# Kernel optimization log

Hardware: AMD Instinct MI355X
Metric: run time of the kernel (lower is better)

The kernel has to match this reference:

```python
import jax, jax.numpy as jnp
import numpy as np

N, IN, H, C, E = 20000, 256, 256, 16, 640000

def sage_conv(x, edge_index, W_l, b_l, W_r):
    # PyG SAGEConv (aggr='mean', root_weight=True):
    # out = lin_l(mean_{j in N(i)} x_j) + lin_r(x_i)
    src, dst = edge_index[0], edge_index[1]
    n = x.shape[0]
    msgs = x[src]                                            # [E, d] irregular gather
    agg = jax.ops.segment_sum(msgs, dst, num_segments=n)     # [N, d]
    deg = jax.ops.segment_sum(jnp.ones((msgs.shape[0],), x.dtype), dst, num_segments=n)
    agg = agg / jnp.maximum(deg, 1.0)[:, None]               # mean aggregation
    return agg @ W_l + b_l + x @ W_r


def setup_inputs() -> dict:
    key = jax.random.key(0)
    ks = jax.random.split(key, 10)
    s = lambda k, fi, fo: jax.random.normal(k, (fi, fo), jnp.float32) / np.sqrt(fi)
    return {
        "x": jax.random.normal(ks[0], (N, IN), jnp.float32),
        "edge_index": jax.random.randint(ks[1], (2, E), 0, N, jnp.int64),
        "W1l": s(ks[2], IN, H), "b1": jnp.zeros((H,), jnp.float32), "W1r": s(ks[3], IN, H),
        "W2l": s(ks[4], H, H),  "b2": jnp.zeros((H,), jnp.float32), "W2r": s(ks[5], H, H),
        "Wc": s(ks[6], H, C),   "bc": jnp.zeros((C,), jnp.float32),
    }


def reference(x, edge_index, W1l, b1, W1r, W2l, b2, W2r, Wc, bc):
    h = sage_conv(x, edge_index, W1l, b1, W1r)
    h = jax.nn.relu(h)                    # dropout is identity in eval mode
    z = sage_conv(h, edge_index, W2l, b2, W2r)
    return z @ Wc + bc                    # classifier logits [N, C]
```

## Files before the change

### kernel.cpp

```cpp
#include <hip/hip_runtime.h>
#include <hip/hip_bf16.h>


#define FEAT 256
#define NCLS 16
#define ZPAD 264
#define CAP  128

typedef __bf16 bf16x8 __attribute__((ext_vector_type(8)));
typedef __bf16 bf16x4 __attribute__((ext_vector_type(4)));
typedef float  f32x4  __attribute__((ext_vector_type(4)));
typedef float  f32x2  __attribute__((ext_vector_type(2)));
typedef unsigned int uint4v __attribute__((ext_vector_type(4)));


__global__ void combo_kernel(const float* __restrict__ x,
                             const float* __restrict__ W1l, const float* __restrict__ W1r,
                             const float* __restrict__ W2l, const float* __restrict__ W2r,
                             const float* __restrict__ Wc, const float* __restrict__ b2,
                             const float* __restrict__ bc,
                             const int* __restrict__ src, const int* __restrict__ dst,
                             __bf16* __restrict__ xb, unsigned char* __restrict__ x8,
                             __bf16* __restrict__ W1lT, __bf16* __restrict__ W1rT,
                             __bf16* __restrict__ WaT, __bf16* __restrict__ WbT,
                             float* __restrict__ bc2,
                             int* __restrict__ cnt, unsigned short* __restrict__ bucket,
                             int n4, int E, int nb_cvt) {
    int t = threadIdx.x;
    int bx = blockIdx.x;
    if (bx < nb_cvt) {
        int i = bx * 256 + t;
        if (i < n4) {
            f32x4 v = ((const f32x4*)x)[i];
            bf16x4 o;
            #pragma unroll
            for (int j = 0; j < 4; ++j) o[j] = (__bf16)v[j];
            ((bf16x4*)xb)[i] = o;
            int pk = 0;
            pk = __builtin_amdgcn_cvt_pk_fp8_f32(v[0], v[1], pk, false);
            pk = __builtin_amdgcn_cvt_pk_fp8_f32(v[2], v[3], pk, true);
            ((int*)x8)[i] = pk;
        }
    } else if (bx < nb_cvt + 512) {
        int b = bx - nb_cvt;
        int w = b >> 8, nn = b & 255;
        const float* W = w ? W1r : W1l;
        __bf16* WT = w ? W1rT : W1lT;
        WT[nn * FEAT + t] = (__bf16)W[t * FEAT + nn];
    } else if (bx < nb_cvt + 512 + 32) {
        int b = bx - nb_cvt - 512;
        int c = b & 15;
        const float* W = (b < 16) ? W2l : W2r;
        __bf16* WT = (b < 16) ? WaT : WbT;
        float s = 0.f;
        #pragma unroll 4
        for (int m = 0; m < FEAT; ++m)
            s += W[t * FEAT + m] * Wc[m * NCLS + c];
        WT[c * FEAT + t] = (__bf16)s;
    } else if (bx == nb_cvt + 512 + 32) {
        if (t < NCLS) {
            float s = 0.f;
            for (int k = 0; k < FEAT; ++k) s += b2[k] * Wc[k * NCLS + t];
            bc2[t] = s + bc[t];
        }
    } else {
        int idx = (bx - nb_cvt - 512 - 33) * 256 + t;
        int e2 = idx * 2;
        if (e2 < E) {
            int2 sv = *(const int2*)(src + e2);
            int2 dv = *(const int2*)(dst + e2);
            int p0 = atomicAdd(&cnt[dv.x], 1);
            if (p0 < CAP) bucket[dv.x * CAP + p0] = (unsigned short)sv.x;
            if (e2 + 1 < E) {
                int p1 = atomicAdd(&cnt[dv.y], 1);
                if (p1 < CAP) bucket[dv.y * CAP + p1] = (unsigned short)sv.y;
            }
        }
    }
}


__global__ __launch_bounds__(256) void agg_fp8_kernel(
    const unsigned char* __restrict__ t8, const int* __restrict__ cnt,
    const unsigned short* __restrict__ bucket, __bf16* __restrict__ out, int n)
{
    int wave = threadIdx.x >> 6;
    int node = blockIdx.x * 4 + wave;
    if (node >= n) return;
    int lane = threadIdx.x & 63;
    int quad = lane >> 4, l16 = lane & 15;
    int c = cnt[node];
    int deg = c < CAP ? c : CAP;
    const unsigned short* lst = bucket + node * CAP;

    f32x4 s0[4], s1[4];
    #pragma unroll
    for (int w = 0; w < 4; ++w) { s0[w] = (f32x4){0.f,0.f,0.f,0.f}; s1[w] = (f32x4){0.f,0.f,0.f,0.f}; }

    int e = quad;
    for (; e + 4 < deg; e += 8) {
        int j0 = lst[e], j1 = lst[e + 4];
        uint4v u0 = *(const uint4v*)(t8 + (size_t)j0 * FEAT + l16 * 16);
        uint4v u1 = *(const uint4v*)(t8 + (size_t)j1 * FEAT + l16 * 16);
        #pragma unroll
        for (int w = 0; w < 4; ++w) {
            f32x2 lo0 = __builtin_amdgcn_cvt_pk_f32_fp8(u0[w], false);
            f32x2 hi0 = __builtin_amdgcn_cvt_pk_f32_fp8(u0[w], true);
            s0[w][0] += lo0[0]; s0[w][1] += lo0[1]; s0[w][2] += hi0[0]; s0[w][3] += hi0[1];
            f32x2 lo1 = __builtin_amdgcn_cvt_pk_f32_fp8(u1[w], false);
            f32x2 hi1 = __builtin_amdgcn_cvt_pk_f32_fp8(u1[w], true);
            s1[w][0] += lo1[0]; s1[w][1] += lo1[1]; s1[w][2] += hi1[0]; s1[w][3] += hi1[1];
        }
    }
    if (e < deg) {
        int j = lst[e];
        uint4v u = *(const uint4v*)(t8 + (size_t)j * FEAT + l16 * 16);
        #pragma unroll
        for (int w = 0; w < 4; ++w) {
            f32x2 lo = __builtin_amdgcn_cvt_pk_f32_fp8(u[w], false);
            f32x2 hi = __builtin_amdgcn_cvt_pk_f32_fp8(u[w], true);
            s0[w][0] += lo[0]; s0[w][1] += lo[1]; s0[w][2] += hi[0]; s0[w][3] += hi[1];
        }
    }

    #pragma unroll
    for (int w = 0; w < 4; ++w)
        #pragma unroll
        for (int j = 0; j < 4; ++j) {
            float v = s0[w][j] + s1[w][j];
            v += __shfl_xor(v, 16, 64);
            v += __shfl_xor(v, 32, 64);
            s0[w][j] = v;
        }

    float inv = (c > 0) ? 1.0f / (float)c : 0.0f;
    bf16x4 o;
    #pragma unroll
    for (int j = 0; j < 4; ++j) o[j] = (__bf16)(s0[quad][j] * inv);
    *(bf16x4*)(out + (size_t)node * FEAT + l16 * 16 + quad * 4) = o;
}


__global__ __launch_bounds__(256) void gemm1_kernel(
    const __bf16* __restrict__ A1, const __bf16* __restrict__ A2,
    const __bf16* __restrict__ B1T, const __bf16* __restrict__ B2T,
    const float* __restrict__ bias,
    const __bf16* __restrict__ WaT, const __bf16* __restrict__ WbT,
    const float* __restrict__ bc2,
    __bf16* __restrict__ pb, float* __restrict__ q, int M)
{
    __shared__ __align__(16) __bf16 tile[32][ZPAD];

    int m0   = blockIdx.x * 32;
    int lane = threadIdx.x & 63;
    int wave = threadIdx.x >> 6;
    int l16  = lane & 15, quad = lane >> 4;

    f32x4 acc[2][4];
    #pragma unroll
    for (int a = 0; a < 2; ++a)
        #pragma unroll
        for (int b = 0; b < 4; ++b) acc[a][b] = (f32x4){0.f, 0.f, 0.f, 0.f};

    int arow[2];
    #pragma unroll
    for (int mt = 0; mt < 2; ++mt) {
        int r = m0 + mt * 16 + l16;
        arow[mt] = (r < M) ? r : (M - 1);
    }
    int nbase = wave * 64;

    for (int pass = 0; pass < 2; ++pass) {
        const __bf16* A  = pass ? A2 : A1;
        const __bf16* BT = pass ? B2T : B1T;
        #pragma unroll 2
        for (int kk = 0; kk < 8; ++kk) {
            int k0 = kk * 32 + quad * 8;
            bf16x8 af[2], bfm[4];
            #pragma unroll
            for (int mt = 0; mt < 2; ++mt)
                af[mt] = *(const bf16x8*)(A + (size_t)arow[mt] * FEAT + k0);
            #pragma unroll
            for (int nt = 0; nt < 4; ++nt)
                bfm[nt] = *(const bf16x8*)(BT + (size_t)(nbase + nt * 16 + l16) * FEAT + k0);
            #pragma unroll
            for (int mt = 0; mt < 2; ++mt)
                #pragma unroll
                for (int nt = 0; nt < 4; ++nt)
                    acc[mt][nt] = __builtin_amdgcn_mfma_f32_16x16x32_bf16(
                        af[mt], bfm[nt], acc[mt][nt], 0, 0, 0);
        }
    }

    #pragma unroll
    for (int nt = 0; nt < 4; ++nt) {
        int col = nbase + nt * 16 + l16;
        float bv = bias[col];
        #pragma unroll
        for (int mt = 0; mt < 2; ++mt) {
            int lr = mt * 16 + quad * 4;
            #pragma unroll
            for (int r = 0; r < 4; ++r) {
                float v = acc[mt][nt][r] + bv;
                tile[lr + r][col] = (__bf16)(v > 0.f ? v : 0.f);
            }
        }
    }
    __syncthreads();

    if (wave < 2) {
        int lr = wave * 16 + l16;
        f32x4 ap = {0.f, 0.f, 0.f, 0.f}, aq = {0.f, 0.f, 0.f, 0.f};
        #pragma unroll
        for (int kk = 0; kk < 8; ++kk) {
            int k0 = kk * 32 + quad * 8;
            bf16x8 a  = *(const bf16x8*)(&tile[lr][k0]);
            bf16x8 ba = *(const bf16x8*)(WaT + (size_t)l16 * FEAT + k0);
            bf16x8 bb = *(const bf16x8*)(WbT + (size_t)l16 * FEAT + k0);
            ap = __builtin_amdgcn_mfma_f32_16x16x32_bf16(a, ba, ap, 0, 0, 0);
            aq = __builtin_amdgcn_mfma_f32_16x16x32_bf16(a, bb, aq, 0, 0, 0);
        }
        float qv = bc2[l16];
        #pragma unroll
        for (int r = 0; r < 4; ++r) {
            int row = m0 + wave * 16 + quad * 4 + r;
            if (row < M) {
                pb[(size_t)row * NCLS + l16] = (__bf16)ap[r];
                q[(size_t)row * NCLS + l16] = aq[r] + qv;
            }
        }
    }
}


__global__ __launch_bounds__(256) void agg_out_kernel(
    const __bf16* __restrict__ pb, const float* __restrict__ q,
    const int* __restrict__ cnt, const unsigned short* __restrict__ bucket,
    float* __restrict__ out, int n)
{
    int wave = threadIdx.x >> 6;
    int node = blockIdx.x * 4 + wave;
    if (node >= n) return;
    int lane = threadIdx.x & 63;
    int quad = lane >> 4, l16 = lane & 15;
    int c = cnt[node];
    int deg = c < CAP ? c : CAP;
    const unsigned short* lst = bucket + node * CAP;

    float s0 = 0.f, s1 = 0.f;
    int e = quad;
    for (; e + 4 < deg; e += 8) {
        int j0 = lst[e], j1 = lst[e + 4];
        s0 += (float)pb[(size_t)j0 * NCLS + l16];
        s1 += (float)pb[(size_t)j1 * NCLS + l16];
    }
    if (e < deg) s0 += (float)pb[(size_t)lst[e] * NCLS + l16];

    float v = s0 + s1;
    v += __shfl_xor(v, 16, 64);
    v += __shfl_xor(v, 32, 64);

    if (quad == 0) {
        float inv = (c > 0) ? 1.0f / (float)c : 0.0f;
        out[(size_t)node * NCLS + l16] = v * inv + q[(size_t)node * NCLS + l16];
    }
}


extern "C" void kernel_launch(void* const* d_in, const int* in_sizes, int n_in,
                              void* d_out, int out_size, void* d_ws, size_t ws_size,
                              hipStream_t stream) {
    const float* x   = (const float*)d_in[0];
    const int*   ei  = (const int*)d_in[1];
    const float* W1l = (const float*)d_in[2];
    const float* b1  = (const float*)d_in[3];
    const float* W1r = (const float*)d_in[4];
    const float* W2l = (const float*)d_in[5];
    const float* b2  = (const float*)d_in[6];
    const float* W2r = (const float*)d_in[7];
    const float* Wc  = (const float*)d_in[8];
    const float* bc  = (const float*)d_in[9];
    float* out = (float*)d_out;

    const int n = in_sizes[0] / FEAT;
    const int E = in_sizes[1] / 2;
    const int* srcp = ei;
    const int* dstp = ei + E;

    char* p = (char*)d_ws;
    auto alloc = [&](size_t bytes) { char* r = p; p += (bytes + 511) & ~511ull; return r; };
    int* cnt       = (int*)alloc((size_t)n * 4);
    unsigned short* bucket = (unsigned short*)alloc((size_t)n * CAP * 2);
    __bf16* W1lT   = (__bf16*)alloc((size_t)FEAT * FEAT * 2);
    __bf16* W1rT   = (__bf16*)alloc((size_t)FEAT * FEAT * 2);
    __bf16* WaT    = (__bf16*)alloc((size_t)NCLS * FEAT * 2);
    __bf16* WbT    = (__bf16*)alloc((size_t)NCLS * FEAT * 2);
    float*  bc2    = (float*)alloc((size_t)NCLS * 4);
    __bf16* xb     = (__bf16*)alloc((size_t)n * FEAT * 2);
    unsigned char* x8 = (unsigned char*)alloc((size_t)n * FEAT);
    __bf16* aggb   = (__bf16*)alloc((size_t)n * FEAT * 2);
    __bf16* pb     = (__bf16*)alloc((size_t)n * NCLS * 2);
    float*  qb     = (float*)alloc((size_t)n * NCLS * 4);

    int n4 = n * FEAT / 4;
    int nb_cvt = (n4 + 255) / 256;
    int nb_edge = (E + 511) / 512;

    hipMemsetAsync(cnt, 0, (size_t)n * 4, stream);

    combo_kernel<<<nb_cvt + 512 + 32 + 1 + nb_edge, 256, 0, stream>>>(
        x, W1l, W1r, W2l, W2r, Wc, b2, bc, srcp, dstp,
        xb, x8, W1lT, W1rT, WaT, WbT, bc2, cnt, bucket, n4, E, nb_cvt);

    agg_fp8_kernel<<<(n + 3) / 4, 256, 0, stream>>>(x8, cnt, bucket, aggb, n);
    gemm1_kernel<<<(n + 31) / 32, 256, 0, stream>>>(aggb, xb, W1lT, W1rT, b1,
                                                    WaT, WbT, bc2, pb, qb, n);

    agg_out_kernel<<<(n + 3) / 4, 256, 0, stream>>>(pb, qb, cnt, bucket, out, n);
}
```

Measured before the change: 199.5 us.

## Reorder combo blocks, vectorize edge bucketing, prefetch neighbor lists via shuffles

The edge-bucketing blocks now come first in the combo kernel and each thread handles four edges with int4 loads and nontemporal bucket stores. Both aggregation kernels load the whole neighbor list once per wave into registers and hand indices out with wave shuffles, unrolling four gathers per iteration for more loads in flight. The tail GEMM epilogue spreads the two 16-class projections across all four waves instead of two. The aim is to cut dependent index-load latency and idle waves, at the cost of extra shuffle instructions and more branches.

After: 214.0 us. 1.07x slower.

```diff
diff --git a/kernel.cpp b/kernel.cpp
--- a/kernel.cpp
+++ b/kernel.cpp
@@ -12,6 +12,15 @@
 typedef float  f32x4  __attribute__((ext_vector_type(4)));
 typedef float  f32x2  __attribute__((ext_vector_type(2)));
 typedef unsigned int uint4v __attribute__((ext_vector_type(4)));
+
+#define ACC8(S, U) do {                                                   \
+    _Pragma("unroll")                                                     \
+    for (int w_ = 0; w_ < 4; ++w_) {                                      \
+        f32x2 lo_ = __builtin_amdgcn_cvt_pk_f32_fp8(U[w_], false);        \
+        f32x2 hi_ = __builtin_amdgcn_cvt_pk_f32_fp8(U[w_], true);         \
+        S[w_][0] += lo_[0]; S[w_][1] += lo_[1];                           \
+        S[w_][2] += hi_[0]; S[w_][3] += hi_[1];                           \
+    } } while (0)
 
 
 __global__ void combo_kernel(const float* __restrict__ x,
@@ -25,11 +34,31 @@
                              __bf16* __restrict__ WaT, __bf16* __restrict__ WbT,
                              float* __restrict__ bc2,
                              int* __restrict__ cnt, unsigned short* __restrict__ bucket,
-                             int n4, int E, int nb_cvt) {
+                             int n4, int E, int nb_edge, int nb_cvt) {
     int t = threadIdx.x;
     int bx = blockIdx.x;
-    if (bx < nb_cvt) {
-        int i = bx * 256 + t;
+    if (bx < nb_edge) {
+        int e4 = (bx * 256 + t) * 4;
+        if (((E & 3) == 0) && e4 + 3 < E) {
+            int4 sv = *(const int4*)(src + e4);
+            int4 dv = *(const int4*)(dst + e4);
+            int p0 = atomicAdd(&cnt[dv.x], 1);
+            int p1 = atomicAdd(&cnt[dv.y], 1);
+            int p2 = atomicAdd(&cnt[dv.z], 1);
+            int p3 = atomicAdd(&cnt[dv.w], 1);
+            if (p0 < CAP) __builtin_nontemporal_store((unsigned short)sv.x, &bucket[(size_t)dv.x * CAP + p0]);
+            if (p1 < CAP) __builtin_nontemporal_store((unsigned short)sv.y, &bucket[(size_t)dv.y * CAP + p1]);
+            if (p2 < CAP) __builtin_nontemporal_store((unsigned short)sv.z, &bucket[(size_t)dv.z * CAP + p2]);
+            if (p3 < CAP) __builtin_nontemporal_store((unsigned short)sv.w, &bucket[(size_t)dv.w * CAP + p3]);
+        } else {
+            for (int k = 0; k < 4 && e4 + k < E; ++k) {
+                int s = src[e4 + k], d = dst[e4 + k];
+                int p = atomicAdd(&cnt[d], 1);
+                if (p < CAP) __builtin_nontemporal_store((unsigned short)s, &bucket[(size_t)d * CAP + p]);
+            }
+        }
+    } else if (bx < nb_edge + nb_cvt) {
+        int i = (bx - nb_edge) * 256 + t;
         if (i < n4) {
             f32x4 v = ((const f32x4*)x)[i];
             bf16x4 o;
@@ -41,14 +70,14 @@
             pk = __builtin_amdgcn_cvt_pk_fp8_f32(v[2], v[3], pk, true);
             ((int*)x8)[i] = pk;
         }
-    } else if (bx < nb_cvt + 512) {
-        int b = bx - nb_cvt;
+    } else if (bx < nb_edge + nb_cvt + 512) {
+        int b = bx - nb_edge - nb_cvt;
         int w = b >> 8, nn = b & 255;
         const float* W = w ? W1r : W1l;
         __bf16* WT = w ? W1rT : W1lT;
         WT[nn * FEAT + t] = (__bf16)W[t * FEAT + nn];
-    } else if (bx < nb_cvt + 512 + 32) {
-        int b = bx - nb_cvt - 512;
+    } else if (bx < nb_edge + nb_cvt + 512 + 32) {
+        int b = bx - nb_edge - nb_cvt - 512;
         int c = b & 15;
         const float* W = (b < 16) ? W2l : W2r;
         __bf16* WT = (b < 16) ? WaT : WbT;
@@ -57,24 +86,11 @@
         for (int m = 0; m < FEAT; ++m)
             s += W[t * FEAT + m] * Wc[m * NCLS + c];
         WT[c * FEAT + t] = (__bf16)s;
-    } else if (bx == nb_cvt + 512 + 32) {
+    } else {
         if (t < NCLS) {
             float s = 0.f;
             for (int k = 0; k < FEAT; ++k) s += b2[k] * Wc[k * NCLS + t];
             bc2[t] = s + bc[t];
-        }
-    } else {
-        int idx = (bx - nb_cvt - 512 - 33) * 256 + t;
-        int e2 = idx * 2;
-        if (e2 < E) {
-            int2 sv = *(const int2*)(src + e2);
-            int2 dv = *(const int2*)(dst + e2);
-            int p0 = atomicAdd(&cnt[dv.x], 1);
-            if (p0 < CAP) bucket[dv.x * CAP + p0] = (unsigned short)sv.x;
-            if (e2 + 1 < E) {
-                int p1 = atomicAdd(&cnt[dv.y], 1);
-                if (p1 < CAP) bucket[dv.y * CAP + p1] = (unsigned short)sv.y;
-            }
         }
     }
 }
@@ -93,33 +109,44 @@
     int deg = c < CAP ? c : CAP;
     const unsigned short* lst = bucket + node * CAP;
 
+    int e0 = 0, e1 = 0;
+    if (lane < deg)      e0 = lst[lane];
+    if (lane + 64 < deg) e1 = lst[lane + 64];
+
     f32x4 s0[4], s1[4];
     #pragma unroll
     for (int w = 0; w < 4; ++w) { s0[w] = (f32x4){0.f,0.f,0.f,0.f}; s1[w] = (f32x4){0.f,0.f,0.f,0.f}; }
 
-    int e = quad;
-    for (; e + 4 < deg; e += 8) {
-        int j0 = lst[e], j1 = lst[e + 4];
-        uint4v u0 = *(const uint4v*)(t8 + (size_t)j0 * FEAT + l16 * 16);
-        uint4v u1 = *(const uint4v*)(t8 + (size_t)j1 * FEAT + l16 * 16);
-        #pragma unroll
-        for (int w = 0; w < 4; ++w) {
-            f32x2 lo0 = __builtin_amdgcn_cvt_pk_f32_fp8(u0[w], false);
-            f32x2 hi0 = __builtin_amdgcn_cvt_pk_f32_fp8(u0[w], true);
-            s0[w][0] += lo0[0]; s0[w][1] += lo0[1]; s0[w][2] += hi0[0]; s0[w][3] += hi0[1];
-            f32x2 lo1 = __builtin_amdgcn_cvt_pk_f32_fp8(u1[w], false);
-            f32x2 hi1 = __builtin_amdgcn_cvt_pk_f32_fp8(u1[w], true);
-            s1[w][0] += lo1[0]; s1[w][1] += lo1[1]; s1[w][2] += hi1[0]; s1[w][3] += hi1[1];
-        }
-    }
-    if (e < deg) {
-        int j = lst[e];
-        uint4v u = *(const uint4v*)(t8 + (size_t)j * FEAT + l16 * 16);
-        #pragma unroll
-        for (int w = 0; w < 4; ++w) {
-            f32x2 lo = __builtin_amdgcn_cvt_pk_f32_fp8(u[w], false);
-            f32x2 hi = __builtin_amdgcn_cvt_pk_f32_fp8(u[w], true);
-            s0[w][0] += lo[0]; s0[w][1] += lo[1]; s0[w][2] += hi[0]; s0[w][3] += hi[1];
+    int nfull = deg >> 2;
+    int rem   = deg & 3;
+    const unsigned char* base = t8 + l16 * 16;
+
+    int tt = 0;
+    for (; tt + 3 < nfull; tt += 4) {
+        int i0 = (tt + 0) * 4 + quad, i1 = (tt + 1) * 4 + quad;
+        int i2 = (tt + 2) * 4 + quad, i3 = (tt + 3) * 4 + quad;
+        int j0 = (i0 < 64) ? __shfl(e0, i0) : __shfl(e1, i0 - 64);
+        int j1 = (i1 < 64) ? __shfl(e0, i1) : __shfl(e1, i1 - 64);
+        int j2 = (i2 < 64) ? __shfl(e0, i2) : __shfl(e1, i2 - 64);
+        int j3 = (i3 < 64) ? __shfl(e0, i3) : __shfl(e1, i3 - 64);
+        uint4v u0 = *(const uint4v*)(base + (size_t)j0 * FEAT);
+        uint4v u1 = *(const uint4v*)(base + (size_t)j1 * FEAT);
+        uint4v u2 = *(const uint4v*)(base + (size_t)j2 * FEAT);
+        uint4v u3 = *(const uint4v*)(base + (size_t)j3 * FEAT);
+        ACC8(s0, u0); ACC8(s1, u1); ACC8(s0, u2); ACC8(s1, u3);
+    }
+    for (; tt < nfull; ++tt) {
+        int i = tt * 4 + quad;
+        int j = (i < 64) ? __shfl(e0, i) : __shfl(e1, i - 64);
+        uint4v u = *(const uint4v*)(base + (size_t)j * FEAT);
+        ACC8(s0, u);
+    }
+    if (rem) {
+        int i = nfull * 4 + quad;
+        int j = (i < 64) ? __shfl(e0, i) : __shfl(e1, i - 64);
+        if (quad < rem) {
+            uint4v u = *(const uint4v*)(base + (size_t)j * FEAT);
+            ACC8(s1, u);
         }
     }
 
@@ -208,25 +235,30 @@
     }
     __syncthreads();
 
-    if (wave < 2) {
-        int lr = wave * 16 + l16;
-        f32x4 ap = {0.f, 0.f, 0.f, 0.f}, aq = {0.f, 0.f, 0.f, 0.f};
+    {
+        int half = wave >> 1;
+        int lr = half * 16 + l16;
+        const __bf16* WT = (wave & 1) ? WbT : WaT;
+        f32x4 a = {0.f, 0.f, 0.f, 0.f};
         #pragma unroll
         for (int kk = 0; kk < 8; ++kk) {
             int k0 = kk * 32 + quad * 8;
-            bf16x8 a  = *(const bf16x8*)(&tile[lr][k0]);
-            bf16x8 ba = *(const bf16x8*)(WaT + (size_t)l16 * FEAT + k0);
-            bf16x8 bb = *(const bf16x8*)(WbT + (size_t)l16 * FEAT + k0);
-            ap = __builtin_amdgcn_mfma_f32_16x16x32_bf16(a, ba, ap, 0, 0, 0);
-            aq = __builtin_amdgcn_mfma_f32_16x16x32_bf16(a, bb, aq, 0, 0, 0);
-        }
-        float qv = bc2[l16];
-        #pragma unroll
-        for (int r = 0; r < 4; ++r) {
-            int row = m0 + wave * 16 + quad * 4 + r;
-            if (row < M) {
-                pb[(size_t)row * NCLS + l16] = (__bf16)ap[r];
-                q[(size_t)row * NCLS + l16] = aq[r] + qv;
+            bf16x8 av = *(const bf16x8*)(&tile[lr][k0]);
+            bf16x8 bv = *(const bf16x8*)(WT + (size_t)l16 * FEAT + k0);
+            a = __builtin_amdgcn_mfma_f32_16x16x32_bf16(av, bv, a, 0, 0, 0);
+        }
+        if (wave & 1) {
+            float qv = bc2[l16];
+            #pragma unroll
+            for (int r = 0; r < 4; ++r) {
+                int row = m0 + half * 16 + quad * 4 + r;
+                if (row < M) q[(size_t)row * NCLS + l16] = a[r] + qv;
+            }
+        } else {
+            #pragma unroll
+            for (int r = 0; r < 4; ++r) {
+                int row = m0 + half * 16 + quad * 4 + r;
+                if (row < M) pb[(size_t)row * NCLS + l16] = (__bf16)a[r];
             }
         }
     }
@@ -247,14 +279,39 @@
     int deg = c < CAP ? c : CAP;
     const unsigned short* lst = bucket + node * CAP;
 
+    int e0 = 0, e1 = 0;
+    if (lane < deg)      e0 = lst[lane];
+    if (lane + 64 < deg) e1 = lst[lane + 64];
+
     float s0 = 0.f, s1 = 0.f;
-    int e = quad;
-    for (; e + 4 < deg; e += 8) {
-        int j0 = lst[e], j1 = lst[e + 4];
-        s0 += (float)pb[(size_t)j0 * NCLS + l16];
-        s1 += (float)pb[(size_t)j1 * NCLS + l16];
-    }
-    if (e < deg) s0 += (float)pb[(size_t)lst[e] * NCLS + l16];
+    int nfull = deg >> 2;
+    int rem   = deg & 3;
+
+    int tt = 0;
+    for (; tt + 3 < nfull; tt += 4) {
+        int i0 = (tt + 0) * 4 + quad, i1 = (tt + 1) * 4 + quad;
+        int i2 = (tt + 2) * 4 + quad, i3 = (tt + 3) * 4 + quad;
+        int j0 = (i0 < 64) ? __shfl(e0, i0) : __shfl(e1, i0 - 64);
+        int j1 = (i1 < 64) ? __shfl(e0, i1) : __shfl(e1, i1 - 64);
+        int j2 = (i2 < 64) ? __shfl(e0, i2) : __shfl(e1, i2 - 64);
+        int j3 = (i3 < 64) ? __shfl(e0, i3) : __shfl(e1, i3 - 64);
+        float v0 = (float)pb[(size_t)j0 * NCLS + l16];
+        float v1 = (float)pb[(size_t)j1 * NCLS + l16];
+        float v2 = (float)pb[(size_t)j2 * NCLS + l16];
+        float v3 = (float)pb[(size_t)j3 * NCLS + l16];
+        s0 += v0 + v1;
+        s1 += v2 + v3;
+    }
+    for (; tt < nfull; ++tt) {
+        int i = tt * 4 + quad;
+        int j = (i < 64) ? __shfl(e0, i) : __shfl(e1, i - 64);
+        s0 += (float)pb[(size_t)j * NCLS + l16];
+    }
+    if (rem) {
+        int i = nfull * 4 + quad;
+        int j = (i < 64) ? __shfl(e0, i) : __shfl(e1, i - 64);
+        if (quad < rem) s1 += (float)pb[(size_t)j * NCLS + l16];
+    }
 
     float v = s0 + s1;
     v += __shfl_xor(v, 16, 64);
@@ -303,14 +360,14 @@
     float*  qb     = (float*)alloc((size_t)n * NCLS * 4);
 
     int n4 = n * FEAT / 4;
-    int nb_cvt = (n4 + 255) / 256;
-    int nb_edge = (E + 511) / 512;
+    int nb_cvt  = (n4 + 255) / 256;
+    int nb_edge = (E + 1023) / 1024;
 
     hipMemsetAsync(cnt, 0, (size_t)n * 4, stream);
 
-    combo_kernel<<<nb_cvt + 512 + 32 + 1 + nb_edge, 256, 0, stream>>>(
+    combo_kernel<<<nb_edge + nb_cvt + 512 + 32 + 1, 256, 0, stream>>>(
         x, W1l, W1r, W2l, W2r, Wc, b2, bc, srcp, dstp,
-        xb, x8, W1lT, W1rT, WaT, WbT, bc2, cnt, bucket, n4, E, nb_cvt);
+        xb, x8, W1lT, W1rT, WaT, WbT, bc2, cnt, bucket, n4, E, nb_edge, nb_cvt);
 
     agg_fp8_kernel<<<(n + 3) / 4, 256, 0, stream>>>(x8, cnt, bucket, aggb, n);
     gemm1_kernel<<<(n + 31) / 32, 256, 0, stream>>>(aggb, xb, W1lT, W1rT, b1,
```
